# Performance work log

Hardware: AMD Instinct MI355X
Metric: run time of the kernel (lower is better)

## Reference

```python
import jax, jax.numpy as jnp
import numpy as np

B, F, H1, H2, C = 8192, 256, 64, 32, 10  # batch, features, hidden1, hidden2, classes


def setup_inputs() -> dict:
    key = jax.random.key(0)
    ks = jax.random.split(key, 7)
    x = jax.random.normal(ks[0], (B, F), dtype=jnp.float32)
    # Per-feature stacked MLP params (xavier-ish scale)
    W1 = jax.random.normal(ks[1], (F, 1, H1), dtype=jnp.float32) * (2.0 / (1 + H1)) ** 0.5
    b1 = jnp.zeros((F, H1), dtype=jnp.float32)
    W2 = jax.random.normal(ks[2], (F, H1, H2), dtype=jnp.float32) * (2.0 / (H1 + H2)) ** 0.5
    b2 = jnp.zeros((F, H2), dtype=jnp.float32)
    Wout = jax.random.normal(ks[3], (F, H2, C), dtype=jnp.float32) * (2.0 / (H2 + C)) ** 0.5
    bias = jnp.zeros((C,), dtype=jnp.float32)
    return {"x": x, "W1": W1, "b1": b1, "W2": W2, "b2": b2, "Wout": Wout, "bias": bias}


def reference(x, W1, b1, W2, b2, Wout, bias):
    # Each feature f gets its own MLP: 1 -> H1 (ReLU) -> H2 (ReLU) -> C (no bias).
    # First layer input is x[:, f] unsqueezed to [B, 1]; since in-dim is 1 it is
    # an outer product: h1[b,f,:] = relu(x[b,f] * W1[f,0,:] + b1[f,:]).
    h1 = jax.nn.relu(x[:, :, None] * W1[:, 0, :][None, :, :] + b1[None, :, :])  # [B,F,H1]
    h2 = jax.nn.relu(jnp.einsum('bfh,fho->bfo', h1, W2) + b2[None, :, :])        # [B,F,H2]
    per_feat = jnp.einsum('bfo,foc->bfc', h2, Wout)                              # [B,F,C]
    # NAM: sum feature contributions + global bias (dropouts are 0 -> identity)
    return per_feat.sum(axis=1) + bias  # [B,C]
```

## Files before the change

### kernel.cpp

```cpp
#include <hip/hip_runtime.h>


#define NB 8192
#define NF 256
#define H1 64
#define H2 32
#define NC 10
#define THREADS 256
#define ROWSPB (THREADS * 2)
#define NRG (NB / ROWSPB)
#define FPG 4
#define NFG (NF / FPG)
#define TS 64

__global__ __launch_bounds__(256) void nam_transpose(const float* __restrict__ x,
                                                     float* __restrict__ xT) {
    __shared__ float tile[TS][TS + 1];
    const int t  = threadIdx.x;
    const int c0 = t & 63;
    const int r0 = t >> 6;
    const int bb = blockIdx.x * TS;
    const int fb = blockIdx.y * TS;
#pragma unroll
    for (int k = 0; k < 16; ++k) {
        const int r = r0 + k * 4;
        tile[r][c0] = x[(size_t)(bb + r) * NF + fb + c0];
    }
    __syncthreads();
#pragma unroll
    for (int k = 0; k < 16; ++k) {
        const int r = r0 + k * 4;
        xT[(size_t)(fb + r) * NB + bb + c0] = tile[c0][r];
    }
}

__global__ __launch_bounds__(THREADS, 4) void nam_core_t(
    const float* __restrict__ xT, const float* __restrict__ W1,
    const float* __restrict__ b1, const float* __restrict__ W2,
    const float* __restrict__ b2, const float* __restrict__ Wout,
    float* __restrict__ partial) {
    const int fg = blockIdx.x;
    const int rg = blockIdx.y;
    const int t  = threadIdx.x;
    const int r0 = rg * ROWSPB + t;
    const int r1 = r0 + THREADS;
    const int f0 = fg * FPG;

    float acc0[NC], acc1[NC];
#pragma unroll
    for (int c = 0; c < NC; ++c) { acc0[c] = 0.f; acc1[c] = 0.f; }

#pragma unroll 1
    for (int ff = 0; ff < FPG; ++ff) {
        const int f = f0 + ff;
        const float xv0 = xT[(size_t)f * NB + r0];
        const float xv1 = xT[(size_t)f * NB + r1];
        const float* __restrict__ W1f = W1 + (size_t)f * H1;
        const float* __restrict__ b1f = b1 + (size_t)f * H1;
        const float* __restrict__ W2f = W2 + (size_t)f * (H1 * H2);
        const float* __restrict__ b2f = b2 + (size_t)f * H2;
        const float* __restrict__ Wof = Wout + (size_t)f * (H2 * NC);

        float h2a[H2], h2b[H2];
#pragma unroll
        for (int o = 0; o < H2; ++o) { const float bb_ = b2f[o]; h2a[o] = bb_; h2b[o] = bb_; }

#pragma unroll 8
        for (int hh = 0; hh < H1; ++hh) {
            const float a0 = fmaxf(fmaf(xv0, W1f[hh], b1f[hh]), 0.f);
            const float a1 = fmaxf(fmaf(xv1, W1f[hh], b1f[hh]), 0.f);
            const float* wr = W2f + (size_t)hh * H2;
#pragma unroll
            for (int o = 0; o < H2; ++o) {
                const float w = wr[o];
                h2a[o] = fmaf(a0, w, h2a[o]);
                h2b[o] = fmaf(a1, w, h2b[o]);
            }
        }

#pragma unroll 8
        for (int o = 0; o < H2; ++o) {
            const float g0 = fmaxf(h2a[o], 0.f), g1 = fmaxf(h2b[o], 0.f);
            const float* wo = Wof + o * NC;
#pragma unroll
            for (int c = 0; c < NC; ++c) {
                const float w = wo[c];
                acc0[c] = fmaf(g0, w, acc0[c]);
                acc1[c] = fmaf(g1, w, acc1[c]);
            }
        }
    }

#pragma unroll
    for (int c = 0; c < NC; ++c) {
        partial[((size_t)fg * NC + c) * NB + r0] = acc0[c];
        partial[((size_t)fg * NC + c) * NB + r1] = acc1[c];
    }
}

__global__ __launch_bounds__(256) void nam_reduce4(const float* __restrict__ part,
                                                   const float* __restrict__ bias,
                                                   float* __restrict__ out) {
    const int i  = blockIdx.x * 256 + threadIdx.x;
    const int c  = i / (NB / 4);
    const int b4 = i % (NB / 4);
    const float bc = bias[c];
    float4 s = {bc, bc, bc, bc};
#pragma unroll 8
    for (int g = 0; g < NFG; ++g) {
        const float4 v = ((const float4*)(part + ((size_t)g * NC + c) * NB))[b4];
        s.x += v.x; s.y += v.y; s.z += v.z; s.w += v.w;
    }
    const int b = 4 * b4;
    out[(size_t)(b + 0) * NC + c] = s.x;
    out[(size_t)(b + 1) * NC + c] = s.y;
    out[(size_t)(b + 2) * NC + c] = s.z;
    out[(size_t)(b + 3) * NC + c] = s.w;
}

__global__ __launch_bounds__(256) void nam_init_out(const float* __restrict__ bias,
                                                    float* __restrict__ out) {
    const int i = blockIdx.x * 256 + threadIdx.x;
    if (i < NB * NC) out[i] = bias[i % NC];
}

__global__ __launch_bounds__(256) void nam_fallback(
    const float* __restrict__ x,  const float* __restrict__ W1,
    const float* __restrict__ b1, const float* __restrict__ W2,
    const float* __restrict__ b2, const float* __restrict__ Wout,
    float* __restrict__ out) {
    const int b  = blockIdx.x * 256 + threadIdx.x;
    const int f0 = blockIdx.y * 16;
    float acc[NC];
#pragma unroll
    for (int c = 0; c < NC; ++c) acc[c] = 0.f;
#pragma unroll 1
    for (int ff = 0; ff < 16; ++ff) {
        const int f = f0 + ff;
        const float xv = x[(size_t)b * NF + f];
        const float* W1f = W1 + (size_t)f * H1;
        const float* b1f = b1 + (size_t)f * H1;
        const float* W2f = W2 + (size_t)f * (H1 * H2);
        const float* b2f = b2 + (size_t)f * H2;
        const float* Wof = Wout + (size_t)f * (H2 * NC);
        float h2[H2];
#pragma unroll
        for (int o = 0; o < H2; ++o) h2[o] = b2f[o];
#pragma unroll 8
        for (int hh = 0; hh < H1; ++hh) {
            const float a = fmaxf(fmaf(xv, W1f[hh], b1f[hh]), 0.f);
            const float* wr = W2f + (size_t)hh * H2;
#pragma unroll
            for (int o = 0; o < H2; ++o) h2[o] = fmaf(a, wr[o], h2[o]);
        }
#pragma unroll
        for (int o = 0; o < H2; ++o) {
            const float g = fmaxf(h2[o], 0.f);
            const float* wo = Wof + o * NC;
#pragma unroll
            for (int c = 0; c < NC; ++c) acc[c] = fmaf(g, wo[c], acc[c]);
        }
    }
    float* orow = out + (size_t)b * NC;
#pragma unroll
    for (int c = 0; c < NC; ++c) atomicAdd(&orow[c], acc[c]);
}

extern "C" void kernel_launch(void* const* d_in, const int* in_sizes, int n_in,
                              void* d_out, int out_size, void* d_ws, size_t ws_size,
                              hipStream_t stream) {
    const float* x    = (const float*)d_in[0];
    const float* W1   = (const float*)d_in[1];
    const float* b1   = (const float*)d_in[2];
    const float* W2   = (const float*)d_in[3];
    const float* b2   = (const float*)d_in[4];
    const float* Wout = (const float*)d_in[5];
    const float* bias = (const float*)d_in[6];
    float* out = (float*)d_out;

    float* xT   = (float*)d_ws;
    float* part = xT + (size_t)NF * NB;
    const size_t need = ((size_t)NF * NB + (size_t)NFG * NC * NB) * sizeof(float);

    if (ws_size >= need) {
        nam_transpose<<<dim3(NB / TS, NF / TS), 256, 0, stream>>>(x, xT);
        nam_core_t<<<dim3(NFG, NRG), THREADS, 0, stream>>>(xT, W1, b1, W2, b2, Wout, part);
        nam_reduce4<<<(NC * NB / 4 + 255) / 256, 256, 0, stream>>>(part, bias, out);
    } else {
        nam_init_out<<<(NB * NC + 255) / 256, 256, 0, stream>>>(bias, out);
        nam_fallback<<<dim3(NB / 256, 16), 256, 0, stream>>>(x, W1, b1, W2, b2, Wout, out);
    }
}
```

Baseline: 180.1 us.

## Drop transpose kernel, load x directly as float4, one row per thread

Removes the separate transpose pass. Each thread now reads the four feature values it needs straight from x with a single float4 load. Each thread handles one batch row instead of two, which doubles the grid, and the occupancy hint rises to 8 blocks per SM. This saves one kernel launch plus the xT write and re-read. The cost is that each weight load is now reused across half as many rows, so weight-load traffic per FMA doubles.

```diff
diff --git a/kernel.cpp b/kernel.cpp
--- a/kernel.cpp
+++ b/kernel.cpp
@@ -7,95 +7,64 @@
 #define H2 32
 #define NC 10
 #define THREADS 256
-#define ROWSPB (THREADS * 2)
-#define NRG (NB / ROWSPB)
 #define FPG 4
 #define NFG (NF / FPG)
-#define TS 64
+#define NRG (NB / THREADS)
 
-__global__ __launch_bounds__(256) void nam_transpose(const float* __restrict__ x,
-                                                     float* __restrict__ xT) {
-    __shared__ float tile[TS][TS + 1];
-    const int t  = threadIdx.x;
-    const int c0 = t & 63;
-    const int r0 = t >> 6;
-    const int bb = blockIdx.x * TS;
-    const int fb = blockIdx.y * TS;
-#pragma unroll
-    for (int k = 0; k < 16; ++k) {
-        const int r = r0 + k * 4;
-        tile[r][c0] = x[(size_t)(bb + r) * NF + fb + c0];
-    }
-    __syncthreads();
-#pragma unroll
-    for (int k = 0; k < 16; ++k) {
-        const int r = r0 + k * 4;
-        xT[(size_t)(fb + r) * NB + bb + c0] = tile[c0][r];
-    }
-}
-
-__global__ __launch_bounds__(THREADS, 4) void nam_core_t(
-    const float* __restrict__ xT, const float* __restrict__ W1,
+__global__ __launch_bounds__(THREADS, 8) void nam_core_g(
+    const float* __restrict__ x,  const float* __restrict__ W1,
     const float* __restrict__ b1, const float* __restrict__ W2,
     const float* __restrict__ b2, const float* __restrict__ Wout,
     float* __restrict__ partial) {
     const int fg = blockIdx.x;
     const int rg = blockIdx.y;
-    const int t  = threadIdx.x;
-    const int r0 = rg * ROWSPB + t;
-    const int r1 = r0 + THREADS;
+    const int b  = rg * THREADS + threadIdx.x;
     const int f0 = fg * FPG;
 
-    float acc0[NC], acc1[NC];
+    const float4 xv4 = *(const float4*)(x + (size_t)b * NF + f0);
+
+    float acc[NC];
 #pragma unroll
-    for (int c = 0; c < NC; ++c) { acc0[c] = 0.f; acc1[c] = 0.f; }
+    for (int c = 0; c < NC; ++c) acc[c] = 0.f;
 
-#pragma unroll 1
-    for (int ff = 0; ff < FPG; ++ff) {
-        const int f = f0 + ff;
-        const float xv0 = xT[(size_t)f * NB + r0];
-        const float xv1 = xT[(size_t)f * NB + r1];
+    auto do_feature = [&](const int f, const float xv) {
         const float* __restrict__ W1f = W1 + (size_t)f * H1;
         const float* __restrict__ b1f = b1 + (size_t)f * H1;
         const float* __restrict__ W2f = W2 + (size_t)f * (H1 * H2);
         const float* __restrict__ b2f = b2 + (size_t)f * H2;
         const float* __restrict__ Wof = Wout + (size_t)f * (H2 * NC);
 
-        float h2a[H2], h2b[H2];
+        float h2[H2];
 #pragma unroll
-        for (int o = 0; o < H2; ++o) { const float bb_ = b2f[o]; h2a[o] = bb_; h2b[o] = bb_; }
+        for (int o = 0; o < H2; ++o) h2[o] = b2f[o];
 
 #pragma unroll 8
         for (int hh = 0; hh < H1; ++hh) {
-            const float a0 = fmaxf(fmaf(xv0, W1f[hh], b1f[hh]), 0.f);
-            const float a1 = fmaxf(fmaf(xv1, W1f[hh], b1f[hh]), 0.f);
+            const float a = fmaxf(fmaf(xv, W1f[hh], b1f[hh]), 0.f);
             const float* wr = W2f + (size_t)hh * H2;
 #pragma unroll
-            for (int o = 0; o < H2; ++o) {
-                const float w = wr[o];
-                h2a[o] = fmaf(a0, w, h2a[o]);
-                h2b[o] = fmaf(a1, w, h2b[o]);
-            }
+            for (int o = 0; o < H2; ++o)
+                h2[o] = fmaf(a, wr[o], h2[o]);
         }
 
 #pragma unroll 8
         for (int o = 0; o < H2; ++o) {
-            const float g0 = fmaxf(h2a[o], 0.f), g1 = fmaxf(h2b[o], 0.f);
+            const float g = fmaxf(h2[o], 0.f);
             const float* wo = Wof + o * NC;
 #pragma unroll
-            for (int c = 0; c < NC; ++c) {
-                const float w = wo[c];
-                acc0[c] = fmaf(g0, w, acc0[c]);
-                acc1[c] = fmaf(g1, w, acc1[c]);
-            }
+            for (int c = 0; c < NC; ++c)
+                acc[c] = fmaf(g, wo[c], acc[c]);
         }
-    }
+    };
+
+    do_feature(f0 + 0, xv4.x);
+    do_feature(f0 + 1, xv4.y);
+    do_feature(f0 + 2, xv4.z);
+    do_feature(f0 + 3, xv4.w);
 
 #pragma unroll
-    for (int c = 0; c < NC; ++c) {
-        partial[((size_t)fg * NC + c) * NB + r0] = acc0[c];
-        partial[((size_t)fg * NC + c) * NB + r1] = acc1[c];
-    }
+    for (int c = 0; c < NC; ++c)
+        partial[((size_t)fg * NC + c) * NB + b] = acc[c];
 }
 
 __global__ __launch_bounds__(256) void nam_reduce4(const float* __restrict__ part,
@@ -178,13 +147,11 @@
     const float* bias = (const float*)d_in[6];
     float* out = (float*)d_out;
 
-    float* xT   = (float*)d_ws;
-    float* part = xT + (size_t)NF * NB;
-    const size_t need = ((size_t)NF * NB + (size_t)NFG * NC * NB) * sizeof(float);
+    float* part = (float*)d_ws;
+    const size_t need = (size_t)NFG * NC * NB * sizeof(float);
 
     if (ws_size >= need) {
-        nam_transpose<<<dim3(NB / TS, NF / TS), 256, 0, stream>>>(x, xT);
-        nam_core_t<<<dim3(NFG, NRG), THREADS, 0, stream>>>(xT, W1, b1, W2, b2, Wout, part);
+        nam_core_g<<<dim3(NFG, NRG), THREADS, 0, stream>>>(x, W1, b1, W2, b2, Wout, part);
         nam_reduce4<<<(NC * NB / 4 + 255) / 256, 256, 0, stream>>>(part, bias, out);
     } else {
         nam_init_out<<<(NB * NC + 255) / 256, 256, 0, stream>>>(bias, out);
```

New measurement: 251.8 us. +39.8%, slower.
